# Kernel tuning notes

Measured on AMD Instinct MI355X. Metric: run time of the kernel, lower is better.

## Reference

```python
import jax, jax.numpy as jnp
import numpy as np
import math

B, L, DIM = 2, 2048, 1024
HEADS = 16
DH = DIM // HEADS  # 64
M_IALSH = 2
U_IALSH = 0.75
NEG = -1e4  # additive mask value for non-matching hash buckets


def setup_inputs() -> dict:
    key = jax.random.key(0)
    k0, k1, k2, k3 = jax.random.split(key, 4)
    return {
        "hidden_states": jax.random.normal(k0, (B, L, DIM), jnp.float32),
        "qk_w": jax.random.normal(k1, (DIM, DIM), jnp.float32) * 0.02,
        "qk_b": jnp.zeros((DIM,), jnp.float32),
        "v_w": jax.random.normal(k2, (DIM, DIM), jnp.float32) * 0.02,
        "v_b": jnp.zeros((DIM,), jnp.float32),
        "hash_a": jax.random.normal(k3, (DH + M_IALSH,), jnp.float32),
    }


def _ialsh_mask(qkh, hash_a):
    # qkh: (b, h, l, dh). IALSH (Improved Asymmetric LSH for MIPS):
    # keys scaled so max norm per (b,h) is U; P(x)=[x, 1/2-||x||^2, 1/2-||x||^4]
    # queries unit-normalized;        Q(x)=[x/||x||, 0, 0]
    norms = jnp.linalg.norm(qkh, axis=-1, keepdims=True)          # (b,h,l,1)
    max_norm = jnp.max(norms, axis=2, keepdims=True)              # (b,h,1,1)
    xk = qkh * (U_IALSH / jnp.maximum(max_norm, 1e-12))
    nk2 = jnp.sum(xk * xk, axis=-1, keepdims=True)                # ||x||^2
    P = jnp.concatenate([xk, 0.5 - nk2, 0.5 - nk2 * nk2], axis=-1)
    q_unit = qkh / jnp.maximum(norms, 1e-12)
    zeros = jnp.zeros_like(nk2)
    Q = jnp.concatenate([q_unit, zeros, zeros], axis=-1)
    hq = (Q @ hash_a) >= 0.0                                      # (b,h,l) sign hash
    hk = (P @ hash_a) >= 0.0
    same = hq[..., :, None] == hk[..., None, :]                   # (b,h,l,l)
    return jnp.where(same, 0.0, NEG).astype(qkh.dtype)


def reference(hidden_states, qk_w, qk_b, v_w, v_b, hash_a):
    b, l, d = hidden_states.shape
    qk = hidden_states @ qk_w.T + qk_b                            # shared Q/K projection
    v = hidden_states @ v_w.T + v_b

    def split(x):  # (b,l,d) -> (b,h,l,dh)
        return x.reshape(b, l, HEADS, DH).transpose(0, 2, 1, 3)

    qkh, vh = split(qk), split(v)
    scores = jnp.einsum('bhqd,bhkd->bhqk', qkh, qkh) / math.sqrt(DH)
    scores = scores + _ialsh_mask(qkh, hash_a)
    probs = jax.nn.softmax(scores, axis=-1)  # dropout = identity (eval mode)
    ctx = jnp.einsum('bhqk,bhkd->bhqd', probs, vh)
    return ctx.transpose(0, 2, 1, 3).reshape(b, l, d)
```

## Files before the change

kernel.cpp:

```cpp
#include <hip/hip_runtime.h>

typedef unsigned short u16;
typedef unsigned char  u8;
typedef unsigned int   u32;
typedef unsigned long long u64;

typedef short bf16x8 __attribute__((ext_vector_type(8)));
typedef float f32x4  __attribute__((ext_vector_type(4)));
typedef float f32x16 __attribute__((ext_vector_type(16)));

#define DEV __device__ __forceinline__

#if __has_builtin(__builtin_amdgcn_exp2f)
#define EXP2(x) __builtin_amdgcn_exp2f(x)
#else
#define EXP2(x) exp2f(x)
#endif

DEV u16 f2bf(float x) {
  u32 u = __builtin_bit_cast(u32, x);
  u32 r = (u + 0x7fffu + ((u >> 16) & 1u)) >> 16;
  return (u16)r;
}
DEV float bf2f(u16 h) {
  u32 u = ((u32)h) << 16;
  return __builtin_bit_cast(float, u);
}
DEV f32x4 mfma16(bf16x8 a, bf16x8 b, f32x4 c) {
  return __builtin_amdgcn_mfma_f32_16x16x32_bf16(a, b, c, 0, 0, 0);
}
DEV f32x16 mfma32(bf16x8 a, bf16x8 b, f32x16 c) {
  return __builtin_amdgcn_mfma_f32_32x32x16_bf16(a, b, c, 0, 0, 0);
}
DEV u32 cvtpk(float lo, float hi) {
  u32 r;
  asm("v_cvt_pk_bf16_f32 %0, %1, %2" : "=v"(r) : "v"(lo), "v"(hi));
  return r;
}
DEV void pswap(u32& x, u32& y) {
  asm("v_permlane32_swap_b32 %0, %1" : "+v"(x), "+v"(y));
}
DEV bf16x8 mkfrag(u32 w0, u32 w1, u32 w2, u32 w3) {
  union { u32 w[4]; bf16x8 v; } u;
  u.w[0] = w0; u.w[1] = w1; u.w[2] = w2; u.w[3] = w3;
  return u.v;
}

#define GLDS(gptr, lptr)                                                  \
  __builtin_amdgcn_global_load_lds(                                       \
      (const __attribute__((address_space(1))) void*)(gptr),              \
      (__attribute__((address_space(3))) void*)(lptr), 16, 0, 0)

__global__ __launch_bounds__(256) void split3_kernel(
    const float* __restrict__ hid, const float* __restrict__ wq,
    const float* __restrict__ wv,
    u16* __restrict__ hHi, u16* __restrict__ hLo,
    u16* __restrict__ wqHi, u16* __restrict__ wqLo, u16* __restrict__ wvHi) {
  const int NH = 4194304, NW = 1048576;
  int i = blockIdx.x * 256 + threadIdx.x;
  if (i < NH) {
    float v = hid[i];
    u16 t = f2bf(v);
    hHi[i] = t;
    hLo[i] = f2bf(v - bf2f(t));
  } else if (i < NH + NW) {
    int j = i - NH;
    float v = wq[j];
    u16 t = f2bf(v);
    wqHi[j] = t;
    wqLo[j] = f2bf(v - bf2f(t));
  } else {
    int j = i - NH - NW;
    wvHi[j] = f2bf(wv[j]);
  }
}

__global__ __launch_bounds__(256) void ca_kernel(
    const float* __restrict__ W, const float* __restrict__ ha, double* __restrict__ ca) {
  int idx = blockIdx.x * 256 + threadIdx.x;
  int h = idx >> 10, k = idx & 1023;
  double s = 0.0;
#pragma unroll 8
  for (int j = 0; j < 64; ++j)
    s += (double)W[(size_t)(h * 64 + j) * 1024 + k] * (double)ha[j];
  ca[idx] = s;
}

__global__ __launch_bounds__(256) void d_kernel(
    const float* __restrict__ hid, const double* __restrict__ ca, float* __restrict__ dq) {
  const int row  = blockIdx.x * 4 + (threadIdx.x >> 6);
  const int lane = threadIdx.x & 63;
  const int b = row >> 11, l = row & 2047;
  double acc[16];
#pragma unroll
  for (int h = 0; h < 16; ++h) acc[h] = 0.0;
  const float* hp = hid + (size_t)row * 1024;
  for (int k = lane; k < 1024; k += 64) {
    const double hv = (double)hp[k];
#pragma unroll
    for (int h = 0; h < 16; ++h) acc[h] += hv * ca[h * 1024 + k];
  }
#pragma unroll
  for (int h = 0; h < 16; ++h) {
    double v = acc[h];
#pragma unroll
    for (int off = 32; off; off >>= 1) v += __shfl_xor(v, off, 64);
    if (lane == 0) dq[(size_t)(b * 16 + h) * 2048 + l] = (float)v;
  }
}

__global__ __launch_bounds__(256, 2) void gemm_fused(
    const u16* __restrict__ hHi, const u16* __restrict__ hLo,
    const u16* __restrict__ wqHi, const u16* __restrict__ wqLo,
    const u16* __restrict__ wvHi,
    const float* __restrict__ qk_b, const float* __restrict__ v_b,
    u16* __restrict__ qkB, u16* __restrict__ vT, float* __restrict__ n2A) {
  constexpr int K = 1024;
  __shared__ u16 S[2][16384];
  const int tid = threadIdx.x, wave = tid >> 6, lane = tid & 63;
  const int quad = lane >> 4, lm = lane & 15;
  const int wr = wave >> 1, wc = wave & 1;
  const int m0 = blockIdx.x * 64, n0 = blockIdx.y * 128;
  const int ch = lane & 3, rA = lane >> 2;

  auto stage = [&](int kt, int buf) {
    const int k0 = kt * 32;
    const int rowA = wave * 16 + rA;
    GLDS(hHi + (size_t)(m0 + rowA) * K + k0 + ch * 8, &S[buf][0 + wave * 512]);
    GLDS(hLo + (size_t)(m0 + rowA) * K + k0 + ch * 8, &S[buf][2048 + wave * 512]);
#pragma unroll
    for (int it = 0; it < 2; ++it) {
      const int rb = wave * 2 + it;
      const int row = rb * 16 + rA;
      GLDS(wqHi + (size_t)(n0 + row) * K + k0 + ch * 8, &S[buf][4096 + rb * 512]);
      GLDS(wqLo + (size_t)(n0 + row) * K + k0 + ch * 8, &S[buf][8192 + rb * 512]);
      GLDS(wvHi + (size_t)(n0 + row) * K + k0 + ch * 8, &S[buf][12288 + rb * 512]);
    }
  };

  f32x4 aq[2][4], av[4][2];
#pragma unroll
  for (int i = 0; i < 2; ++i)
#pragma unroll
    for (int j = 0; j < 4; ++j) aq[i][j] = {0.f, 0.f, 0.f, 0.f};
#pragma unroll
  for (int i = 0; i < 4; ++i)
#pragma unroll
    for (int j = 0; j < 2; ++j) av[i][j] = {0.f, 0.f, 0.f, 0.f};

  stage(0, 0);
  __syncthreads();

  for (int kt = 0; kt < 32; ++kt) {
    const int cur = kt & 1;
    if (kt < 31) stage(kt + 1, cur ^ 1);

    bf16x8 a_h[2], a_l[2], b_h[4], b_l[4], w_h[4];
#pragma unroll
    for (int i = 0; i < 2; ++i) {
      a_h[i] = *(const bf16x8*)&S[cur][(wr * 32 + i * 16 + lm) * 32 + quad * 8];
      a_l[i] = *(const bf16x8*)&S[cur][2048 + (wr * 32 + i * 16 + lm) * 32 + quad * 8];
    }
#pragma unroll
    for (int j = 0; j < 4; ++j) {
      b_h[j] = *(const bf16x8*)&S[cur][4096 + (wc * 64 + j * 16 + lm) * 32 + quad * 8];
      b_l[j] = *(const bf16x8*)&S[cur][8192 + (wc * 64 + j * 16 + lm) * 32 + quad * 8];
      w_h[j] = *(const bf16x8*)&S[cur][12288 + (wc * 64 + j * 16 + lm) * 32 + quad * 8];
    }
#pragma unroll
    for (int i = 0; i < 2; ++i)
#pragma unroll
      for (int j = 0; j < 4; ++j) {
        aq[i][j] = mfma16(a_h[i], b_h[j], aq[i][j]);
        aq[i][j] = mfma16(a_h[i], b_l[j], aq[i][j]);
        aq[i][j] = mfma16(a_l[i], b_h[j], aq[i][j]);
      }
#pragma unroll
    for (int iv = 0; iv < 4; ++iv)
#pragma unroll
      for (int jv = 0; jv < 2; ++jv)
        av[iv][jv] = mfma16(w_h[iv], a_h[jv], av[iv][jv]);

    __syncthreads();
  }

  const int hidx = blockIdx.y * 2 + wc;
#pragma unroll
  for (int i = 0; i < 2; ++i) {
    float nn[4] = {0.f, 0.f, 0.f, 0.f};
#pragma unroll
    for (int j = 0; j < 4; ++j) {
      const int col = n0 + wc * 64 + j * 16 + lm;
      const float bv = qk_b[col];
#pragma unroll
      for (int r = 0; r < 4; ++r) {
        const int row = m0 + wr * 32 + i * 16 + quad * 4 + r;
        const float val = aq[i][j][r] + bv;
        qkB[(size_t)row * 1024 + col] = f2bf(val);
        nn[r] += val * val;
      }
    }
#pragma unroll
    for (int r = 0; r < 4; ++r)
#pragma unroll
      for (int off = 1; off < 16; off <<= 1) nn[r] += __shfl_xor(nn[r], off, 64);
    if (lm == 0) {
      const int row = m0 + wr * 32 + i * 16 + quad * 4;
      const int b = row >> 11, l = row & 2047;
      *(float4*)&n2A[(size_t)(b * 16 + hidx) * 2048 + l] =
          make_float4(nn[0], nn[1], nn[2], nn[3]);
    }
  }
#pragma unroll
  for (int iv = 0; iv < 4; ++iv)
#pragma unroll
    for (int r = 0; r < 4; ++r) {
      const int vcol = n0 + wc * 64 + iv * 16 + quad * 4 + r;
      const float bv = v_b[vcol];
#pragma unroll
      for (int jv = 0; jv < 2; ++jv) {
        const int tok = m0 + wr * 32 + jv * 16 + lm;
        vT[(size_t)vcol * 4096 + tok] = f2bf(av[iv][jv][r] + bv);
      }
    }
}

__global__ __launch_bounds__(256) void bits_kernel(
    const float* __restrict__ n2A, const float* __restrict__ dq,
    const float* __restrict__ ha, u8* __restrict__ hqA, u64* __restrict__ hkM) {
  const int bh = blockIdx.x;
  const int tid = threadIdx.x;
  const int wave = tid >> 6, lane = tid & 63;
  __shared__ float red[4];
  const float* n2p = n2A + (size_t)bh * 2048;
  float4 v0 = ((const float4*)n2p)[tid];
  float4 v1 = ((const float4*)n2p)[tid + 256];
  float lmax = fmaxf(fmaxf(fmaxf(v0.x, v0.y), fmaxf(v0.z, v0.w)),
                     fmaxf(fmaxf(v1.x, v1.y), fmaxf(v1.z, v1.w)));
#pragma unroll
  for (int off = 1; off < 64; off <<= 1) lmax = fmaxf(lmax, __shfl_xor(lmax, off, 64));
  if (lane == 0) red[wave] = lmax;
  __syncthreads();
  const float maxn2 = fmaxf(fmaxf(red[0], red[1]), fmaxf(red[2], red[3]));
  const float s = 0.75f / fmaxf(sqrtf(maxn2), 1e-12f);
  const float a64 = ha[64], a65 = ha[65];
#pragma unroll
  for (int it = 0; it < 8; ++it) {
    const int l = it * 256 + tid;
    const float dv = dq[(size_t)bh * 2048 + l];
    const float n2 = n2p[l];
    const float nk2 = s * s * n2;
    const float hkdot = s * dv + (0.5f - nk2) * a64 + (0.5f - nk2 * nk2) * a65;
    hqA[(size_t)bh * 2048 + l] = (dv >= 0.f) ? 1 : 0;
    const u64 m = __ballot(hkdot >= 0.f);
    if (lane == 0) hkM[(size_t)bh * 32 + it * 4 + wave] = m;
  }
}

__global__ __launch_bounds__(256, 2) void attn_kernel(
    const u16* __restrict__ qkb, const u16* __restrict__ vT,
    const u8* __restrict__ hqA, const u64* __restrict__ hkM,
    float* __restrict__ out) {
  __shared__ u16 Ks[2][4096];
  __shared__ u16 Vs[2][4096];

  const int id = blockIdx.x;
  const int bh = id & 31, qt = id >> 5;
  const int b = bh >> 4, h = bh & 15;
  const int tid = threadIdx.x, wave = tid >> 6, lane = tid & 63;
  const int col = lane & 31;
  const int hf = lane >> 5;
  const int ch7 = col & 7;
  const int r8 = lane >> 3, ch = lane & 7;
  const int q0 = qt * 128;
  const int token = q0 + wave * 32 + col;

  const u16* qbase = qkb + (size_t)b * 2048 * 1024 + h * 64;
  const u16* vtb = vT + (size_t)h * 64 * 4096 + b * 2048;
  const u64* hkp = hkM + (size_t)bh * 32;

  bf16x8 aQ[4];
#pragma unroll
  for (int c = 0; c < 4; ++c)
    aQ[c] = *(const bf16x8*)(qbase + (size_t)token * 1024 + c * 16 + hf * 8);
  const u32 hqx = hqA[(size_t)bh * 2048 + token] ? 0xFFFFFFFFu : 0u;

  const int srow = wave * 16;
  auto stage = [&](int kt, int buf) {
#pragma unroll
    for (int i = 0; i < 2; ++i) {
      const int row = srow + i * 8 + r8;
      const int sw = (ch ^ (row & 7)) * 8;
      GLDS(qbase + (size_t)(kt * 64 + row) * 1024 + sw, &Ks[buf][(srow + i * 8) * 64]);
      GLDS(vtb + (size_t)row * 4096 + kt * 64 + sw, &Vs[buf][(srow + i * 8) * 64]);
    }
  };

  f32x16 acc[2];
#pragma unroll
  for (int d = 0; d < 2; ++d)
#pragma unroll
    for (int r = 0; r < 16; ++r) acc[d][r] = 0.f;
  float accL = 0.f;

  const float SCL = 0.18033688f;
  const float M0 = -4.3280854f;

  u64 mk = hkp[0];
  stage(0, 0);
  __syncthreads();

  for (int kt = 0; kt < 32; ++kt) {
    const int cur = kt & 1;
    if (kt < 31) stage(kt + 1, cur ^ 1);
    const u64 mk_next = (kt < 31) ? hkp[kt + 1] : 0ull;

    const u64 msh = mk >> (hf * 4);
    u32 mw[2];
    mw[0] = (u32)msh;
    mw[1] = (u32)(msh >> 32);

#pragma unroll
    for (int kb = 0; kb < 2; ++kb) {
      const u32 hw = mw[kb] ^ hqx;
      f32x16 cs;
#pragma unroll
      for (int r = 0; r < 16; ++r) cs[r] = 0.f;
      __builtin_amdgcn_s_setprio(1);
#pragma unroll
      for (int c = 0; c < 4; ++c) {
        const bf16x8 aK = *(const bf16x8*)
            &Ks[cur][(kb * 32 + col) * 64 + (((c * 2 + hf) ^ ch7) * 8)];
        cs = mfma32(aK, aQ[c], cs);
      }
      __builtin_amdgcn_s_setprio(0);

      float pv[16];
#pragma unroll
      for (int r = 0; r < 16; ++r) {
        const int pos = (r & 3) + 8 * (r >> 2);
        float p = EXP2(__builtin_fmaf(cs[r], SCL, M0));
        p = ((hw >> pos) & 1u) ? 0.f : p;
        accL += p;
        pv[r] = p;
      }
      u32 pk[8];
#pragma unroll
      for (int i = 0; i < 8; ++i) pk[i] = cvtpk(pv[2 * i], pv[2 * i + 1]);
      pswap(pk[0], pk[2]);
      pswap(pk[1], pk[3]);
      pswap(pk[4], pk[6]);
      pswap(pk[5], pk[7]);
      const bf16x8 fr0 = mkfrag(pk[0], pk[1], pk[2], pk[3]);
      const bf16x8 fr1 = mkfrag(pk[4], pk[5], pk[6], pk[7]);

      __builtin_amdgcn_s_setprio(1);
#pragma unroll
      for (int db = 0; db < 2; ++db) {
        const bf16x8 aV0 = *(const bf16x8*)
            &Vs[cur][(db * 32 + col) * 64 + ((((kb * 2 + 0) * 2 + hf) ^ ch7) * 8)];
        acc[db] = mfma32(aV0, fr0, acc[db]);
        const bf16x8 aV1 = *(const bf16x8*)
            &Vs[cur][(db * 32 + col) * 64 + ((((kb * 2 + 1) * 2 + hf) ^ ch7) * 8)];
        acc[db] = mfma32(aV1, fr1, acc[db]);
      }
      __builtin_amdgcn_s_setprio(0);
    }

    mk = mk_next;
    __syncthreads();
  }

  accL += __shfl_xor(accL, 32);
  const float inv = 1.0f / accL;
  float* op = out + (size_t)(b * 2048 + token) * 1024 + h * 64 + hf * 4;
#pragma unroll
  for (int db = 0; db < 2; ++db)
#pragma unroll
    for (int g = 0; g < 4; ++g) {
      float4 v4 = make_float4(acc[db][g * 4 + 0] * inv, acc[db][g * 4 + 1] * inv,
                              acc[db][g * 4 + 2] * inv, acc[db][g * 4 + 3] * inv);
      *(float4*)(op + db * 32 + g * 8) = v4;
    }
}

extern "C" void kernel_launch(void* const* d_in, const int* in_sizes, int n_in,
                              void* d_out, int out_size, void* d_ws, size_t ws_size,
                              hipStream_t stream) {
  const float* hidden = (const float*)d_in[0];
  const float* qk_w   = (const float*)d_in[1];
  const float* qk_b   = (const float*)d_in[2];
  const float* v_w    = (const float*)d_in[3];
  const float* v_b    = (const float*)d_in[4];
  const float* hash_a = (const float*)d_in[5];
  float* out = (float*)d_out;

  char* base = (char*)d_ws;
  size_t off = 0;
  auto take = [&](size_t bytes) -> char* {
    char* r = base + off;
    off += (bytes + 255) & ~(size_t)255;
    return r;
  };
  const size_t NH = 4194304;
  const size_t NW = 1048576;
  u16* hHi  = (u16*)take(NH * 2);
  u16* hLo  = (u16*)take(NH * 2);
  u16* wqHi = (u16*)take(NW * 2);
  u16* wqLo = (u16*)take(NW * 2);
  u16* wvHi = (u16*)take(NW * 2);
  u16* qkB  = (u16*)take(NH * 2);
  u16* vT   = (u16*)take(NH * 2);
  double* ca = (double*)take(16 * 1024 * 8);
  float* dq  = (float*)take(65536 * 4);
  float* n2A = (float*)take(65536 * 4);
  u8* hqA = (u8*)take(65536);
  u64* hkM = (u64*)take(32 * 32 * 8);

  hipLaunchKernelGGL(split3_kernel, dim3((NH + 2 * NW) / 256), dim3(256), 0, stream,
                     hidden, qk_w, v_w, hHi, hLo, wqHi, wqLo, wvHi);
  hipLaunchKernelGGL(ca_kernel, dim3(64), dim3(256), 0, stream, qk_w, hash_a, ca);
  hipLaunchKernelGGL(d_kernel, dim3(1024), dim3(256), 0, stream, hidden, ca, dq);
  hipLaunchKernelGGL(gemm_fused, dim3(64, 8), dim3(256), 0, stream,
                     hHi, hLo, wqHi, wqLo, wvHi, qk_b, v_b, qkB, vT, n2A);
  hipLaunchKernelGGL(bits_kernel, dim3(32), dim3(256), 0, stream, n2A, dq, hash_a, hqA, hkM);
  hipLaunchKernelGGL(attn_kernel, dim3(512), dim3(256), 0, stream, qkB, vT, hqA, hkM, out);
}
```

Measured before the change: 228.6 us.

## Shrink attention blocks, compute row sums via MFMA, double rows in d_kernel

The attention kernel now uses 128-thread blocks covering 64 query rows, with twice as many blocks, so each wave stages more K/V rows. The softmax denominator is accumulated with an extra MFMA against a ones fragment instead of scalar adds plus a cross-lane shuffle, and the s_setprio hints are dropped. Separately, d_kernel has each wave process two rows so every ca load is reused twice, halving its grid. The MFMA row-sum sums bf16-rounded probabilities, which slightly changes numerics, and the smaller attention blocks give less K/V reuse per staged tile.

```diff
diff --git a/kernel.cpp b/kernel.cpp
--- a/kernel.cpp
+++ b/kernel.cpp
@@ -88,24 +88,36 @@
 
 __global__ __launch_bounds__(256) void d_kernel(
     const float* __restrict__ hid, const double* __restrict__ ca, float* __restrict__ dq) {
-  const int row  = blockIdx.x * 4 + (threadIdx.x >> 6);
+  const int row0 = blockIdx.x * 8 + (threadIdx.x >> 6) * 2;
   const int lane = threadIdx.x & 63;
-  const int b = row >> 11, l = row & 2047;
-  double acc[16];
-#pragma unroll
-  for (int h = 0; h < 16; ++h) acc[h] = 0.0;
-  const float* hp = hid + (size_t)row * 1024;
+  double a0[16], a1[16];
+#pragma unroll
+  for (int h = 0; h < 16; ++h) { a0[h] = 0.0; a1[h] = 0.0; }
+  const float* hp = hid + (size_t)row0 * 1024;
   for (int k = lane; k < 1024; k += 64) {
-    const double hv = (double)hp[k];
-#pragma unroll
-    for (int h = 0; h < 16; ++h) acc[h] += hv * ca[h * 1024 + k];
+    const double h0 = (double)hp[k];
+    const double h1 = (double)hp[k + 1024];
+#pragma unroll
+    for (int h = 0; h < 16; ++h) {
+      const double c = ca[h * 1024 + k];
+      a0[h] += h0 * c;
+      a1[h] += h1 * c;
+    }
   }
 #pragma unroll
   for (int h = 0; h < 16; ++h) {
-    double v = acc[h];
-#pragma unroll
-    for (int off = 32; off; off >>= 1) v += __shfl_xor(v, off, 64);
-    if (lane == 0) dq[(size_t)(b * 16 + h) * 2048 + l] = (float)v;
+    double v0 = a0[h], v1 = a1[h];
+#pragma unroll
+    for (int off = 32; off; off >>= 1) {
+      v0 += __shfl_xor(v0, off, 64);
+      v1 += __shfl_xor(v1, off, 64);
+    }
+    if (lane == 0) {
+      const int b0 = row0 >> 11, l0 = row0 & 2047;
+      dq[(size_t)(b0 * 16 + h) * 2048 + l0] = (float)v0;
+      const int r1 = row0 + 1;
+      dq[(size_t)((r1 >> 11) * 16 + h) * 2048 + (r1 & 2047)] = (float)v1;
+    }
   }
 }
 
@@ -257,7 +269,7 @@
   }
 }
 
-__global__ __launch_bounds__(256, 2) void attn_kernel(
+__global__ __launch_bounds__(128, 2) void attn_kernel(
     const u16* __restrict__ qkb, const u16* __restrict__ vT,
     const u8* __restrict__ hqA, const u64* __restrict__ hkM,
     float* __restrict__ out) {
@@ -272,7 +284,7 @@
   const int hf = lane >> 5;
   const int ch7 = col & 7;
   const int r8 = lane >> 3, ch = lane & 7;
-  const int q0 = qt * 128;
+  const int q0 = qt * 64;
   const int token = q0 + wave * 32 + col;
 
   const u16* qbase = qkb + (size_t)b * 2048 * 1024 + h * 64;
@@ -285,10 +297,10 @@
     aQ[c] = *(const bf16x8*)(qbase + (size_t)token * 1024 + c * 16 + hf * 8);
   const u32 hqx = hqA[(size_t)bh * 2048 + token] ? 0xFFFFFFFFu : 0u;
 
-  const int srow = wave * 16;
+  const int srow = wave * 32;
   auto stage = [&](int kt, int buf) {
 #pragma unroll
-    for (int i = 0; i < 2; ++i) {
+    for (int i = 0; i < 4; ++i) {
       const int row = srow + i * 8 + r8;
       const int sw = (ch ^ (row & 7)) * 8;
       GLDS(qbase + (size_t)(kt * 64 + row) * 1024 + sw, &Ks[buf][(srow + i * 8) * 64]);
@@ -297,11 +309,10 @@
   };
 
   f32x16 acc[2];
-#pragma unroll
-  for (int d = 0; d < 2; ++d)
-#pragma unroll
-    for (int r = 0; r < 16; ++r) acc[d][r] = 0.f;
-  float accL = 0.f;
+  f32x16 accLv;
+#pragma unroll
+  for (int r = 0; r < 16; ++r) { acc[0][r] = 0.f; acc[1][r] = 0.f; accLv[r] = 0.f; }
+  const bf16x8 ones = {0x3F80, 0x3F80, 0x3F80, 0x3F80, 0x3F80, 0x3F80, 0x3F80, 0x3F80};
 
   const float SCL = 0.18033688f;
   const float M0 = -4.3280854f;
@@ -326,27 +337,24 @@
       f32x16 cs;
 #pragma unroll
       for (int r = 0; r < 16; ++r) cs[r] = 0.f;
-      __builtin_amdgcn_s_setprio(1);
 #pragma unroll
       for (int c = 0; c < 4; ++c) {
         const bf16x8 aK = *(const bf16x8*)
             &Ks[cur][(kb * 32 + col) * 64 + (((c * 2 + hf) ^ ch7) * 8)];
         cs = mfma32(aK, aQ[c], cs);
       }
-      __builtin_amdgcn_s_setprio(0);
-
-      float pv[16];
-#pragma unroll
-      for (int r = 0; r < 16; ++r) {
-        const int pos = (r & 3) + 8 * (r >> 2);
-        float p = EXP2(__builtin_fmaf(cs[r], SCL, M0));
-        p = ((hw >> pos) & 1u) ? 0.f : p;
-        accL += p;
-        pv[r] = p;
-      }
       u32 pk[8];
 #pragma unroll
-      for (int i = 0; i < 8; ++i) pk[i] = cvtpk(pv[2 * i], pv[2 * i + 1]);
+      for (int i = 0; i < 8; ++i) {
+        const int r0 = 2 * i, r1 = 2 * i + 1;
+        const int pos0 = (r0 & 3) + 8 * (r0 >> 2);
+        const int pos1 = (r1 & 3) + 8 * (r1 >> 2);
+        float p0 = EXP2(__builtin_fmaf(cs[r0], SCL, M0));
+        float p1 = EXP2(__builtin_fmaf(cs[r1], SCL, M0));
+        p0 = ((hw >> pos0) & 1u) ? 0.f : p0;
+        p1 = ((hw >> pos1) & 1u) ? 0.f : p1;
+        pk[i] = cvtpk(p0, p1);
+      }
       pswap(pk[0], pk[2]);
       pswap(pk[1], pk[3]);
       pswap(pk[4], pk[6]);
@@ -354,7 +362,9 @@
       const bf16x8 fr0 = mkfrag(pk[0], pk[1], pk[2], pk[3]);
       const bf16x8 fr1 = mkfrag(pk[4], pk[5], pk[6], pk[7]);
 
-      __builtin_amdgcn_s_setprio(1);
+      accLv = mfma32(ones, fr0, accLv);
+      accLv = mfma32(ones, fr1, accLv);
+
 #pragma unroll
       for (int db = 0; db < 2; ++db) {
         const bf16x8 aV0 = *(const bf16x8*)
@@ -364,15 +374,13 @@
             &Vs[cur][(db * 32 + col) * 64 + ((((kb * 2 + 1) * 2 + hf) ^ ch7) * 8)];
         acc[db] = mfma32(aV1, fr1, acc[db]);
       }
-      __builtin_amdgcn_s_setprio(0);
     }
 
     mk = mk_next;
     __syncthreads();
   }
 
-  accL += __shfl_xor(accL, 32);
-  const float inv = 1.0f / accL;
+  const float inv = 1.0f / accLv[0];
   float* op = out + (size_t)(b * 2048 + token) * 1024 + h * 64 + hf * 4;
 #pragma unroll
   for (int db = 0; db < 2; ++db)
@@ -420,9 +428,9 @@
   hipLaunchKernelGGL(split3_kernel, dim3((NH + 2 * NW) / 256), dim3(256), 0, stream,
                      hidden, qk_w, v_w, hHi, hLo, wqHi, wqLo, wvHi);
   hipLaunchKernelGGL(ca_kernel, dim3(64), dim3(256), 0, stream, qk_w, hash_a, ca);
-  hipLaunchKernelGGL(d_kernel, dim3(1024), dim3(256), 0, stream, hidden, ca, dq);
+  hipLaunchKernelGGL(d_kernel, dim3(512), dim3(256), 0, stream, hidden, ca, dq);
   hipLaunchKernelGGL(gemm_fused, dim3(64, 8), dim3(256), 0, stream,
                      hHi, hLo, wqHi, wqLo, wvHi, qk_b, v_b, qkB, vT, n2A);
   hipLaunchKernelGGL(bits_kernel, dim3(32), dim3(256), 0, stream, n2A, dq, hash_a, hqA, hkM);
-  hipLaunchKernelGGL(attn_kernel, dim3(512), dim3(256), 0, stream, qkB, vT, hqA, hkM, out);
-}
+  hipLaunchKernelGGL(attn_kernel, dim3(1024), dim3(128), 0, stream, qkB, vT, hqA, hkM, out);
+}
```

New measurement: 223.3 us. 1.02x faster.
